# Performance work log

Measured on AMD Instinct MI355X. Metric: run time of the kernel, lower is better.

Reference implementation:

```python
import jax, jax.numpy as jnp
import numpy as np

N, DX1, DX2, DH = 16384, 1024, 1024, 2048


def _linear_params(key, din, dout):
    kw, kb = jax.random.split(key)
    bound = 1.0 / np.sqrt(din)
    W = jax.random.uniform(kw, (din, dout), jnp.float32, -bound, bound)
    b = jax.random.uniform(kb, (dout,), jnp.float32, -bound, bound)
    return W, b


def setup_inputs() -> dict:
    key = jax.random.key(0)
    ks = jax.random.split(key, 8)
    X1 = jax.random.normal(ks[0], (N, DX1), jnp.float32)
    X2 = jax.random.normal(ks[1], (N, DX2), jnp.float32)
    Y = jax.random.normal(ks[2], (N, 1), jnp.float32)
    w1h_W, w1h_b = _linear_params(ks[3], DX1, DH)
    w2h_W, w2h_b = _linear_params(ks[4], DX2, DH)
    wh1_W, wh1_b = _linear_params(ks[5], DH, DX1)
    wh2_W, wh2_b = _linear_params(ks[6], DH, DX2)
    who_W, who_b = _linear_params(ks[7], DH, 1)
    return dict(X1=X1, X2=X2, Y=Y,
                w1h_W=w1h_W, w1h_b=w1h_b, w2h_W=w2h_W, w2h_b=w2h_b,
                wh1_W=wh1_W, wh1_b=wh1_b, wh2_W=wh2_W, wh2_b=wh2_b,
                who_W=who_W, who_b=who_b)


def _row_sqnorm(x):
    # algebraic rewrite of torch.diag(x @ x.T): per-row sum of squares, shape [N, 1]
    return jnp.sum(x * x, axis=1, keepdims=True)


def reference(X1, X2, Y, w1h_W, w1h_b, w2h_W, w2h_b,
              wh1_W, wh1_b, wh2_W, wh2_b, who_W, who_b):
    lin = lambda x, W, b: x @ W + b
    H1 = lin(X1, w1h_W, w1h_b)              # [N, DH]
    H2 = lin(X2, w2h_W, w2h_b)              # [N, DH]
    X2p = lin(H1, wh2_W, wh2_b)             # [N, DX2]
    X1p = lin(H2, wh1_W, wh1_b)             # [N, DX1]
    L1 = _row_sqnorm(X2p - X2)              # [N, 1]
    L2 = _row_sqnorm(X1p - X1)
    L3 = _row_sqnorm(H1 - H2)
    L4 = lin(H1 + H2, who_W, who_b) * 0.5 - Y  # [N, 1]
    # loss = sum of squares of each per-row term (Li.T @ Li)
    loss = (jnp.sum(L1 * L1) + jnp.sum(L2 * L2)
            + jnp.sum(L3 * L3) + jnp.sum(L4 * L4))
    return loss
```

## Files before the change

kernel.cpp:

```cpp
#include <hip/hip_runtime.h>
#include <cstdint>
#include <cstddef>

#define NR 16384
#define DX 1024
#define DH 2048

typedef unsigned short u16;
typedef _Float16 half8 __attribute__((ext_vector_type(8)));
typedef _Float16 half4v __attribute__((ext_vector_type(4)));
typedef float f32x4 __attribute__((ext_vector_type(4)));

__device__ __forceinline__ u16 f2h_bits(float v) {
    union { _Float16 h; u16 u; } c;
    c.h = (_Float16)v;
    return c.u;
}

__device__ __forceinline__ void gl_lds16(const void* g, void* l) {
    __builtin_amdgcn_global_load_lds(
        (const __attribute__((address_space(1))) void*)g,
        (__attribute__((address_space(3))) void*)l, 16, 0, 0);
}

__global__ __launch_bounds__(256) void cast_f32_f16(const float* __restrict__ in,
                                                    u16* __restrict__ out) {
    size_t i = ((size_t)blockIdx.x * 256 + threadIdx.x) * 4;
    float4 v = *(const float4*)&in[i];
    half4v o = { (_Float16)v.x, (_Float16)v.y, (_Float16)v.z, (_Float16)v.w };
    *(half4v*)&out[i] = o;
}

__global__ __launch_bounds__(256) void transpose_cast(const float* __restrict__ in,
                                                      u16* __restrict__ out,
                                                      int K, int D) {
    __shared__ float tile[32][33];
    int tx = threadIdx.x & 31;
    int ty = threadIdx.x >> 5;
    int d0 = blockIdx.x * 32, k0 = blockIdx.y * 32;
#pragma unroll
    for (int i = 0; i < 32; i += 8)
        tile[ty + i][tx] = in[(size_t)(k0 + ty + i) * D + d0 + tx];
    __syncthreads();
#pragma unroll
    for (int i = 0; i < 32; i += 8)
        out[(size_t)(d0 + ty + i) * K + k0 + tx] = f2h_bits(tile[tx][ty + i]);
}

template <int MODE>
__global__ __launch_bounds__(512, 2) void gemm256(
    const u16* __restrict__ A, const u16* __restrict__ Bt,
    const float* __restrict__ bias,
    u16* __restrict__ C, const float* __restrict__ Xref,
    float* __restrict__ Lacc,
    int M, int N, int K) {
    __shared__ __align__(16) u16 As[2][16384];
    __shared__ __align__(16) u16 Bs[2][16384];

    const int nwg = gridDim.x;
    const int bid = blockIdx.x;
    const int cpx = nwg >> 3;
    const int wg  = (bid & 7) * cpx + (bid >> 3);
    const int NBN = N >> 8;
    const int m0 = (wg / NBN) * 256;
    const int n0 = (wg % NBN) * 256;

    const int tid  = threadIdx.x;
    const int lane = tid & 63;
    const int w    = tid >> 6;
    const int wr   = w >> 2;
    const int wn   = w & 3;
    const int fr   = lane & 15;
    const int qa   = (lane >> 4) * 8;
    const int NT   = K >> 6;

    f32x4 acc[8][4] = {};

    const int sxh   = ((fr >> 2) & 1) << 4;
    const int aoff0 = (((wr * 128 + fr) * 64) + qa) ^ sxh;
    const int boff0 = (((wn * 64 + fr) * 64) + qa) ^ sxh;

    const int stg_c = (((tid & 7) ^ (((tid >> 5) & 1) << 1))) << 3;
    const int stg_r = tid >> 3;
    const int stg_w = (tid >> 6) << 9;

#define STAGE(G, ldK, rowbase, kt, lbase, half_idx)                            \
    do {                                                                       \
        const u16* _s = (G) + (size_t)((rowbase) + (half_idx) * 128 + stg_r) * \
                                  (ldK) + (kt) * 64 + stg_c;                   \
        u16* _d = (lbase) + (half_idx) * 8192 + stg_w;                         \
        gl_lds16(_s, _d);                                                      \
        gl_lds16(_s + (size_t)64 * (ldK), _d + 4096);                          \
    } while (0)

#define MFMA_(d, av, bv) \
    d = __builtin_amdgcn_mfma_f32_16x16x32_f16(av, bv, d, 0, 0, 0)

    STAGE(A, K, m0, 0, &As[0][0], 0);
    STAGE(Bt, K, n0, 0, &Bs[0][0], 0);
    STAGE(A, K, m0, 0, &As[0][0], 1);
    STAGE(Bt, K, n0, 0, &Bs[0][0], 1);
    STAGE(Bt, K, n0, 1, &Bs[1][0], 0);
    STAGE(A, K, m0, 1, &As[1][0], 0);
    asm volatile("s_waitcnt vmcnt(4)" ::: "memory");
    __builtin_amdgcn_s_barrier();

    for (int t = 0; t < NT; ++t) {
        const int bb = t & 1;
        const u16* Ab = &As[bb][0];
        const u16* Bb = &Bs[bb][0];
        u16* Acur = &As[bb][0];
        u16* Bcur = &Bs[bb][0];
        u16* Anx  = &As[bb ^ 1][0];
        u16* Bnx  = &Bs[bb ^ 1][0];
        half8 af[4][2], bf[4][2];

#pragma unroll
        for (int m = 0; m < 4; ++m)
#pragma unroll
            for (int ks = 0; ks < 2; ++ks)
                af[m][ks] = *(const half8*)&Ab[aoff0 + m * 1024 + ks * 32];
#pragma unroll
        for (int n = 0; n < 2; ++n)
#pragma unroll
            for (int ks = 0; ks < 2; ++ks)
                bf[n][ks] = *(const half8*)&Bb[boff0 + n * 1024 + ks * 32];
        if (t + 1 < NT) STAGE(A, K, m0, t + 1, Anx, 1);
        __builtin_amdgcn_s_barrier();
        asm volatile("s_waitcnt lgkmcnt(0)" ::: "memory");
        __builtin_amdgcn_s_setprio(1);
#pragma unroll
        for (int m = 0; m < 4; ++m)
#pragma unroll
            for (int n = 0; n < 2; ++n)
#pragma unroll
                for (int ks = 0; ks < 2; ++ks)
                    MFMA_(acc[m][n], af[m][ks], bf[n][ks]);
        __builtin_amdgcn_s_setprio(0);
        __builtin_amdgcn_s_barrier();

#pragma unroll
        for (int n = 2; n < 4; ++n)
#pragma unroll
            for (int ks = 0; ks < 2; ++ks)
                bf[n][ks] = *(const half8*)&Bb[boff0 + n * 1024 + ks * 32];
        if (t + 1 < NT) STAGE(Bt, K, n0, t + 1, Bnx, 1);
        __builtin_amdgcn_s_barrier();
        asm volatile("s_waitcnt lgkmcnt(0)" ::: "memory");
        __builtin_amdgcn_s_setprio(1);
#pragma unroll
        for (int m = 0; m < 4; ++m)
#pragma unroll
            for (int n = 2; n < 4; ++n)
#pragma unroll
                for (int ks = 0; ks < 2; ++ks)
                    MFMA_(acc[m][n], af[m][ks], bf[n][ks]);
        __builtin_amdgcn_s_setprio(0);
        __builtin_amdgcn_s_barrier();

#pragma unroll
        for (int m = 0; m < 4; ++m)
#pragma unroll
            for (int ks = 0; ks < 2; ++ks)
                af[m][ks] = *(const half8*)&Ab[aoff0 + 4096 + m * 1024 + ks * 32];
        if (t + 2 < NT) STAGE(Bt, K, n0, t + 2, Bcur, 0);
        __builtin_amdgcn_s_barrier();
        asm volatile("s_waitcnt lgkmcnt(0)" ::: "memory");
        __builtin_amdgcn_s_setprio(1);
#pragma unroll
        for (int m = 0; m < 4; ++m)
#pragma unroll
            for (int n = 0; n < 2; ++n)
#pragma unroll
                for (int ks = 0; ks < 2; ++ks)
                    MFMA_(acc[4 + m][n], af[m][ks], bf[n][ks]);
        __builtin_amdgcn_s_setprio(0);
        __builtin_amdgcn_s_barrier();

        if (t + 2 < NT) STAGE(A, K, m0, t + 2, Acur, 0);
        __builtin_amdgcn_s_barrier();
        __builtin_amdgcn_s_setprio(1);
#pragma unroll
        for (int m = 0; m < 4; ++m)
#pragma unroll
            for (int n = 2; n < 4; ++n)
#pragma unroll
                for (int ks = 0; ks < 2; ++ks)
                    MFMA_(acc[4 + m][n], af[m][ks], bf[n][ks]);
        __builtin_amdgcn_s_setprio(0);
        if (t + 2 < NT)
            asm volatile("s_waitcnt vmcnt(4)" ::: "memory");
        else
            asm volatile("s_waitcnt vmcnt(0)" ::: "memory");
        __builtin_amdgcn_s_barrier();
    }

    const int colbase = n0 + wn * 64 + fr;
    float bj[4];
#pragma unroll
    for (int j = 0; j < 4; ++j) bj[j] = bias[colbase + j * 16];

    if (MODE == 0) {
#pragma unroll
        for (int i = 0; i < 8; ++i) {
            int rowb = m0 + wr * 128 + i * 16 + (lane >> 4) * 4;
#pragma unroll
            for (int r = 0; r < 4; ++r) {
                size_t ro = (size_t)(rowb + r) * N;
#pragma unroll
                for (int j = 0; j < 4; ++j)
                    C[ro + colbase + j * 16] = f2h_bits(acc[i][j][r] + bj[j]);
            }
        }
    } else {
#pragma unroll
        for (int i = 0; i < 8; ++i) {
            int rowb = m0 + wr * 128 + i * 16 + (lane >> 4) * 4;
#pragma unroll
            for (int r = 0; r < 4; ++r) {
                size_t ro = (size_t)(rowb + r) * N;
                float s = 0.f;
#pragma unroll
                for (int j = 0; j < 4; ++j) {
                    float d = acc[i][j][r] + bj[j] - Xref[ro + colbase + j * 16];
                    s += d * d;
                }
                s += __shfl_xor(s, 1, 64);
                s += __shfl_xor(s, 2, 64);
                s += __shfl_xor(s, 4, 64);
                s += __shfl_xor(s, 8, 64);
                if (fr == 0) atomicAdd(&Lacc[rowb + r], s);
            }
        }
    }
#undef STAGE
#undef MFMA_
}

__global__ __launch_bounds__(256) void l34_kernel(
    const u16* __restrict__ H1, const u16* __restrict__ H2,
    const float* __restrict__ whoW,
    float* __restrict__ L3, float* __restrict__ L4) {
    int row = blockIdx.x;
    int tid = threadIdx.x;
    const half8 h1 = *(const half8*)&H1[(size_t)row * DH + tid * 8];
    const half8 h2 = *(const half8*)&H2[(size_t)row * DH + tid * 8];
    float4 w0 = *(const float4*)&whoW[tid * 8];
    float4 w1 = *(const float4*)&whoW[tid * 8 + 4];
    float wv[8] = { w0.x, w0.y, w0.z, w0.w, w1.x, w1.y, w1.z, w1.w };
    float s3 = 0.f, s4 = 0.f;
#pragma unroll
    for (int u = 0; u < 8; ++u) {
        float a = (float)h1[u], b = (float)h2[u];
        float d = a - b;
        s3 += d * d;
        s4 += (a + b) * wv[u];
    }
#pragma unroll
    for (int off = 1; off < 64; off <<= 1) {
        s3 += __shfl_xor(s3, off, 64);
        s4 += __shfl_xor(s4, off, 64);
    }
    __shared__ float sm[8];
    int wvi = tid >> 6, ln = tid & 63;
    if (ln == 0) { sm[wvi] = s3; sm[4 + wvi] = s4; }
    __syncthreads();
    if (tid == 0) {
        L3[row] = sm[0] + sm[1] + sm[2] + sm[3];
        L4[row] = sm[4] + sm[5] + sm[6] + sm[7];
    }
}

__global__ __launch_bounds__(1024) void final_reduce(
    const float* __restrict__ L1, const float* __restrict__ L2,
    const float* __restrict__ L3, const float* __restrict__ L4,
    const float* __restrict__ Y, const float* __restrict__ whob,
    float* __restrict__ out) {
    float s = 0.f;
    float wb = whob[0];
    for (int r = threadIdx.x; r < NR; r += 1024) {
        float l4 = 0.5f * (L4[r] + wb) - Y[r];
        s += L1[r] * L1[r] + L2[r] * L2[r] + L3[r] * L3[r] + l4 * l4;
    }
#pragma unroll
    for (int off = 1; off < 64; off <<= 1) s += __shfl_xor(s, off, 64);
    __shared__ float sm[16];
    int w = threadIdx.x >> 6, ln = threadIdx.x & 63;
    if (ln == 0) sm[w] = s;
    __syncthreads();
    if (threadIdx.x == 0) {
        float t = 0.f;
#pragma unroll
        for (int i = 0; i < 16; ++i) t += sm[i];
        out[0] = t;
    }
}

extern "C" void kernel_launch(void* const* d_in, const int* in_sizes, int n_in,
                              void* d_out, int out_size, void* d_ws, size_t ws_size,
                              hipStream_t stream) {
    const float* X1   = (const float*)d_in[0];
    const float* X2   = (const float*)d_in[1];
    const float* Y    = (const float*)d_in[2];
    const float* w1hW = (const float*)d_in[3];
    const float* w1hb = (const float*)d_in[4];
    const float* w2hW = (const float*)d_in[5];
    const float* w2hb = (const float*)d_in[6];
    const float* wh1W = (const float*)d_in[7];
    const float* wh1b = (const float*)d_in[8];
    const float* wh2W = (const float*)d_in[9];
    const float* wh2b = (const float*)d_in[10];
    const float* whoW = (const float*)d_in[11];
    const float* whob = (const float*)d_in[12];

    char* ws = (char*)d_ws;
    u16* X1h  = (u16*)(ws);
    u16* X2h  = X1h + (size_t)NR * DX;
    u16* H1h  = X2h + (size_t)NR * DX;
    u16* H2h  = H1h + (size_t)NR * DH;
    u16* w1hT = H2h + (size_t)NR * DH;
    u16* w2hT = w1hT + (size_t)DH * DX;
    u16* wh1T = w2hT + (size_t)DH * DX;
    u16* wh2T = wh1T + (size_t)DX * DH;
    float* L1a = (float*)(wh2T + (size_t)DX * DH);
    float* L2a = L1a + NR;
    float* L3a = L2a + NR;
    float* L4a = L3a + NR;

    hipMemsetAsync(L1a, 0, 2 * (size_t)NR * sizeof(float), stream);

    cast_f32_f16<<<NR * DX / 1024, 256, 0, stream>>>(X1, X1h);
    cast_f32_f16<<<NR * DX / 1024, 256, 0, stream>>>(X2, X2h);
    transpose_cast<<<dim3(DH / 32, DX / 32), 256, 0, stream>>>(w1hW, w1hT, DX, DH);
    transpose_cast<<<dim3(DH / 32, DX / 32), 256, 0, stream>>>(w2hW, w2hT, DX, DH);
    transpose_cast<<<dim3(DX / 32, DH / 32), 256, 0, stream>>>(wh1W, wh1T, DH, DX);
    transpose_cast<<<dim3(DX / 32, DH / 32), 256, 0, stream>>>(wh2W, wh2T, DH, DX);

    gemm256<0><<<dim3((NR / 256) * (DH / 256)), 512, 0, stream>>>(
        X1h, w1hT, w1hb, H1h, nullptr, nullptr, NR, DH, DX);
    gemm256<0><<<dim3((NR / 256) * (DH / 256)), 512, 0, stream>>>(
        X2h, w2hT, w2hb, H2h, nullptr, nullptr, NR, DH, DX);

    l34_kernel<<<NR, 256, 0, stream>>>(H1h, H2h, whoW, L3a, L4a);

    gemm256<1><<<dim3((NR / 256) * (DX / 256)), 512, 0, stream>>>(
        H1h, wh2T, wh2b, nullptr, X2, L1a, NR, DX, DH);
    gemm256<1><<<dim3((NR / 256) * (DX / 256)), 512, 0, stream>>>(
        H2h, wh1T, wh1b, nullptr, X1, L2a, NR, DX, DH);

    final_reduce<<<1, 1024, 0, stream>>>(L1a, L2a, L3a, L4a, Y, whob, (float*)d_out);
}
```

Baseline: 570.5 us.

## Fuse L3/L4 row reductions into second GEMM epilogue and widen LDS swizzle

Removes the separate l34_kernel by computing the H1-H2 squared difference and the who projection inside the H2 GEMM epilogue, reading H1 back and accumulating per-row partials with atomics. This avoids a second full pass over H1 and H2 from memory. The LDS swizzle also changes from a 1-bit XOR to a 3-bit XOR on both the staging and fragment-read sides, meant to cut bank conflicts. The costs are extra uncoalesced 2-byte H1 reads and more atomics in that epilogue, plus float reduction order that now varies between runs.

```diff
diff --git a/kernel.cpp b/kernel.cpp
--- a/kernel.cpp
+++ b/kernel.cpp
@@ -15,6 +15,12 @@
     union { _Float16 h; u16 u; } c;
     c.h = (_Float16)v;
     return c.u;
+}
+
+__device__ __forceinline__ float h2f_bits(u16 v) {
+    union { u16 u; _Float16 h; } c;
+    c.u = v;
+    return (float)c.h;
 }
 
 __device__ __forceinline__ void gl_lds16(const void* g, void* l) {
@@ -53,6 +59,8 @@
     const float* __restrict__ bias,
     u16* __restrict__ C, const float* __restrict__ Xref,
     float* __restrict__ Lacc,
+    const u16* __restrict__ Hoth, const float* __restrict__ Wo,
+    float* __restrict__ L4o,
     int M, int N, int K) {
     __shared__ __align__(16) u16 As[2][16384];
     __shared__ __align__(16) u16 Bs[2][16384];
@@ -76,11 +84,15 @@
 
     f32x4 acc[8][4] = {};
 
-    const int sxh   = ((fr >> 2) & 1) << 4;
-    const int aoff0 = (((wr * 128 + fr) * 64) + qa) ^ sxh;
-    const int boff0 = (((wn * 64 + fr) * 64) + qa) ^ sxh;
-
-    const int stg_c = (((tid & 7) ^ (((tid >> 5) & 1) << 1))) << 3;
+    const int sx = (fr & 7) << 3;
+    int aofK[2], bofK[2];
+#pragma unroll
+    for (int ks = 0; ks < 2; ++ks) {
+        aofK[ks] = (((wr * 128 + fr) * 64) + qa + ks * 32) ^ sx;
+        bofK[ks] = (((wn * 64 + fr) * 64) + qa + ks * 32) ^ sx;
+    }
+
+    const int stg_c = ((tid & 7) ^ ((tid >> 3) & 7)) << 3;
     const int stg_r = tid >> 3;
     const int stg_w = (tid >> 6) << 9;
 
@@ -119,12 +131,12 @@
         for (int m = 0; m < 4; ++m)
 #pragma unroll
             for (int ks = 0; ks < 2; ++ks)
-                af[m][ks] = *(const half8*)&Ab[aoff0 + m * 1024 + ks * 32];
+                af[m][ks] = *(const half8*)&Ab[aofK[ks] + m * 1024];
 #pragma unroll
         for (int n = 0; n < 2; ++n)
 #pragma unroll
             for (int ks = 0; ks < 2; ++ks)
-                bf[n][ks] = *(const half8*)&Bb[boff0 + n * 1024 + ks * 32];
+                bf[n][ks] = *(const half8*)&Bb[bofK[ks] + n * 1024];
         if (t + 1 < NT) STAGE(A, K, m0, t + 1, Anx, 1);
         __builtin_amdgcn_s_barrier();
         asm volatile("s_waitcnt lgkmcnt(0)" ::: "memory");
@@ -143,7 +155,7 @@
         for (int n = 2; n < 4; ++n)
 #pragma unroll
             for (int ks = 0; ks < 2; ++ks)
-                bf[n][ks] = *(const half8*)&Bb[boff0 + n * 1024 + ks * 32];
+                bf[n][ks] = *(const half8*)&Bb[bofK[ks] + n * 1024];
         if (t + 1 < NT) STAGE(Bt, K, n0, t + 1, Bnx, 1);
         __builtin_amdgcn_s_barrier();
         asm volatile("s_waitcnt lgkmcnt(0)" ::: "memory");
@@ -162,7 +174,7 @@
         for (int m = 0; m < 4; ++m)
 #pragma unroll
             for (int ks = 0; ks < 2; ++ks)
-                af[m][ks] = *(const half8*)&Ab[aoff0 + 4096 + m * 1024 + ks * 32];
+                af[m][ks] = *(const half8*)&Ab[aofK[ks] + 4096 + m * 1024];
         if (t + 2 < NT) STAGE(Bt, K, n0, t + 2, Bcur, 0);
         __builtin_amdgcn_s_barrier();
         asm volatile("s_waitcnt lgkmcnt(0)" ::: "memory");
@@ -212,7 +224,7 @@
                     C[ro + colbase + j * 16] = f2h_bits(acc[i][j][r] + bj[j]);
             }
         }
-    } else {
+    } else if (MODE == 1) {
 #pragma unroll
         for (int i = 0; i < 8; ++i) {
             int rowb = m0 + wr * 128 + i * 16 + (lane >> 4) * 4;
@@ -232,43 +244,43 @@
                 if (fr == 0) atomicAdd(&Lacc[rowb + r], s);
             }
         }
+    } else {
+        float wj[4];
+#pragma unroll
+        for (int j = 0; j < 4; ++j) wj[j] = Wo[colbase + j * 16];
+#pragma unroll
+        for (int i = 0; i < 8; ++i) {
+            int rowb = m0 + wr * 128 + i * 16 + (lane >> 4) * 4;
+#pragma unroll
+            for (int r = 0; r < 4; ++r) {
+                size_t ro = (size_t)(rowb + r) * N;
+                float s3 = 0.f, s4 = 0.f;
+#pragma unroll
+                for (int j = 0; j < 4; ++j) {
+                    float h2 = acc[i][j][r] + bj[j];
+                    C[ro + colbase + j * 16] = f2h_bits(h2);
+                    float h1 = h2f_bits(Hoth[ro + colbase + j * 16]);
+                    float d = h1 - h2;
+                    s3 += d * d;
+                    s4 += (h1 + h2) * wj[j];
+                }
+                s3 += __shfl_xor(s3, 1, 64);
+                s3 += __shfl_xor(s3, 2, 64);
+                s3 += __shfl_xor(s3, 4, 64);
+                s3 += __shfl_xor(s3, 8, 64);
+                s4 += __shfl_xor(s4, 1, 64);
+                s4 += __shfl_xor(s4, 2, 64);
+                s4 += __shfl_xor(s4, 4, 64);
+                s4 += __shfl_xor(s4, 8, 64);
+                if (fr == 0) {
+                    atomicAdd(&Lacc[rowb + r], s3);
+                    atomicAdd(&L4o[rowb + r], s4);
+                }
+            }
+        }
     }
 #undef STAGE
 #undef MFMA_
-}
-
-__global__ __launch_bounds__(256) void l34_kernel(
-    const u16* __restrict__ H1, const u16* __restrict__ H2,
-    const float* __restrict__ whoW,
-    float* __restrict__ L3, float* __restrict__ L4) {
-    int row = blockIdx.x;
-    int tid = threadIdx.x;
-    const half8 h1 = *(const half8*)&H1[(size_t)row * DH + tid * 8];
-    const half8 h2 = *(const half8*)&H2[(size_t)row * DH + tid * 8];
-    float4 w0 = *(const float4*)&whoW[tid * 8];
-    float4 w1 = *(const float4*)&whoW[tid * 8 + 4];
-    float wv[8] = { w0.x, w0.y, w0.z, w0.w, w1.x, w1.y, w1.z, w1.w };
-    float s3 = 0.f, s4 = 0.f;
-#pragma unroll
-    for (int u = 0; u < 8; ++u) {
-        float a = (float)h1[u], b = (float)h2[u];
-        float d = a - b;
-        s3 += d * d;
-        s4 += (a + b) * wv[u];
-    }
-#pragma unroll
-    for (int off = 1; off < 64; off <<= 1) {
-        s3 += __shfl_xor(s3, off, 64);
-        s4 += __shfl_xor(s4, off, 64);
-    }
-    __shared__ float sm[8];
-    int wvi = tid >> 6, ln = tid & 63;
-    if (ln == 0) { sm[wvi] = s3; sm[4 + wvi] = s4; }
-    __syncthreads();
-    if (tid == 0) {
-        L3[row] = sm[0] + sm[1] + sm[2] + sm[3];
-        L4[row] = sm[4] + sm[5] + sm[6] + sm[7];
-    }
 }
 
 __global__ __launch_bounds__(1024) void final_reduce(
@@ -327,7 +339,7 @@
     float* L3a = L2a + NR;
     float* L4a = L3a + NR;
 
-    hipMemsetAsync(L1a, 0, 2 * (size_t)NR * sizeof(float), stream);
+    hipMemsetAsync(L1a, 0, 4 * (size_t)NR * sizeof(float), stream);
 
     cast_f32_f16<<<NR * DX / 1024, 256, 0, stream>>>(X1, X1h);
     cast_f32_f16<<<NR * DX / 1024, 256, 0, stream>>>(X2, X2h);
@@ -337,16 +349,18 @@
     transpose_cast<<<dim3(DX / 32, DH / 32), 256, 0, stream>>>(wh2W, wh2T, DH, DX);
 
     gemm256<0><<<dim3((NR / 256) * (DH / 256)), 512, 0, stream>>>(
-        X1h, w1hT, w1hb, H1h, nullptr, nullptr, NR, DH, DX);
-    gemm256<0><<<dim3((NR / 256) * (DH / 256)), 512, 0, stream>>>(
-        X2h, w2hT, w2hb, H2h, nullptr, nullptr, NR, DH, DX);
-
-    l34_kernel<<<NR, 256, 0, stream>>>(H1h, H2h, whoW, L3a, L4a);
+        X1h, w1hT, w1hb, H1h, nullptr, nullptr, nullptr, nullptr, nullptr,
+        NR, DH, DX);
+    gemm256<2><<<dim3((NR / 256) * (DH / 256)), 512, 0, stream>>>(
+        X2h, w2hT, w2hb, H2h, nullptr, L3a, H1h, whoW, L4a,
+        NR, DH, DX);
 
     gemm256<1><<<dim3((NR / 256) * (DX / 256)), 512, 0, stream>>>(
-        H1h, wh2T, wh2b, nullptr, X2, L1a, NR, DX, DH);
+        H1h, wh2T, wh2b, nullptr, X2, L1a, nullptr, nullptr, nullptr,
+        NR, DX, DH);
     gemm256<1><<<dim3((NR / 256) * (DX / 256)), 512, 0, stream>>>(
-        H2h, wh1T, wh1b, nullptr, X1, L2a, NR, DX, DH);
+        H2h, wh1T, wh1b, nullptr, X1, L2a, nullptr, nullptr, nullptr,
+        NR, DX, DH);
 
     final_reduce<<<1, 1024, 0, stream>>>(L1a, L2a, L3a, L4a, Y, whob, (float*)d_out);
 }
```

New measurement: 558.9 us. -2.0%, faster.
